# Kernel optimization log

Measured on AMD Instinct MI355X. Metric: run time of the kernel, lower is better.

Reference implementation:

```python
import jax, jax.numpy as jnp
import numpy as np

B, L, D, H, FF = 2, 4096, 512, 8, 2048
HD = D // H
EPS = 1e-5


def _layer_norm(x, g, b):
    mu = jnp.mean(x, axis=-1, keepdims=True)
    var = jnp.mean(jnp.square(x - mu), axis=-1, keepdims=True)
    return (x - mu) * jax.lax.rsqrt(var + EPS) * g + b


def setup_inputs() -> dict:
    key = jax.random.key(0)
    ks = jax.random.split(key, 16)
    s = 1.0 / np.sqrt(D)
    inp = {
        'x': jax.random.normal(ks[0], (B, L, D), dtype=jnp.float32),
        'Wq': jax.random.normal(ks[1], (D, D), dtype=jnp.float32) * s,
        'bq': jnp.zeros((D,), jnp.float32),
        'Wk': jax.random.normal(ks[2], (D, D), dtype=jnp.float32) * s,
        'bk': jnp.zeros((D,), jnp.float32),
        'Wv': jax.random.normal(ks[3], (D, D), dtype=jnp.float32) * s,
        'bv': jnp.zeros((D,), jnp.float32),
        'Wo': jax.random.normal(ks[4], (D, D), dtype=jnp.float32) * s,
        'bo': jnp.zeros((D,), jnp.float32),
        'ln1_g': jnp.ones((D,), jnp.float32),
        'ln1_b': jnp.zeros((D,), jnp.float32),
        'W1': jax.random.normal(ks[5], (D, FF), dtype=jnp.float32) * s,
        'b1': jnp.zeros((FF,), jnp.float32),
        'W2': jax.random.normal(ks[6], (FF, D), dtype=jnp.float32) * (1.0 / np.sqrt(FF)),
        'b2': jnp.zeros((D,), jnp.float32),
        'ln2_g': jnp.ones((D,), jnp.float32),
        'ln2_b': jnp.zeros((D,), jnp.float32),
        'window': 128,
    }
    return inp


def reference(x, Wq, bq, Wk, bk, Wv, bv, Wo, bo, ln1_g, ln1_b, W1, b1, W2, b2, ln2_g, ln2_b, window):
    # ---- local (banded) self-attention, matching nn.MultiheadAttention math ----
    q = (x @ Wq + bq).reshape(B, L, H, HD)
    k = (x @ Wk + bk).reshape(B, L, H, HD)
    v = (x @ Wv + bv).reshape(B, L, H, HD)
    scale = 1.0 / np.sqrt(HD)
    scores = jnp.einsum('bqhd,bkhd->bhqk', q, k) * scale  # [B,H,L,L]
    idx = jnp.arange(L)
    band = jnp.abs(idx[None, :] - idx[:, None]) > window   # True = masked
    scores = jnp.where(band[None, None], -jnp.inf, scores)
    probs = jax.nn.softmax(scores, axis=-1)
    attn = jnp.einsum('bhqk,bkhd->bqhd', probs, v).reshape(B, L, D)
    attn = attn @ Wo + bo
    # ---- residual + norm1 ----
    h = _layer_norm(x + attn, ln1_g, ln1_b)
    # ---- FFN + residual + norm2 (dropout=0 at eval) ----
    ff = jax.nn.relu(h @ W1 + b1) @ W2 + b2
    return _layer_norm(h + ff, ln2_g, ln2_b)
```

## Files before the change

kernel.cpp:

```cpp
#include <hip/hip_runtime.h>

namespace {

constexpr int B = 2, L = 4096, D = 512, H = 8, FF = 2048;
constexpr int M = B * L;
constexpr float LN_EPS = 1e-5f;

typedef __attribute__((ext_vector_type(8))) short short8;
typedef __attribute__((ext_vector_type(4))) float floatx4;

typedef __attribute__((address_space(3))) unsigned int lds_uint;
typedef const __attribute__((address_space(1))) unsigned int glob_uint;

__device__ __forceinline__ void gl_lds16(const unsigned short* g, unsigned short* l) {
  __builtin_amdgcn_global_load_lds((glob_uint*)g, (lds_uint*)l, 16, 0, 0);
}

__device__ __forceinline__ unsigned short f2bf(float f) {
  union { float f; unsigned u; } v; v.f = f;
  unsigned r = v.u + 0x7FFFu + ((v.u >> 16) & 1u);
  return (unsigned short)(r >> 16);
}

__device__ __forceinline__ float bf2f(unsigned short b) {
  union { unsigned u; float f; } v; v.u = ((unsigned)b) << 16;
  return v.f;
}

__global__ __launch_bounds__(256)
void k_prep(const float* __restrict__ x,
            const float* __restrict__ Wq, const float* __restrict__ Wk,
            const float* __restrict__ Wv, const float* __restrict__ Wo,
            const float* __restrict__ W1, const float* __restrict__ W2,
            const float* __restrict__ bq, const float* __restrict__ bk,
            const float* __restrict__ bv,
            unsigned short* __restrict__ Xb,
            unsigned short* __restrict__ WqkvT, unsigned short* __restrict__ WoT,
            unsigned short* __restrict__ W1T, unsigned short* __restrict__ W2T,
            float* __restrict__ bqkv) {
  __shared__ unsigned short tile[64 * 72];
  if (blockIdx.x < 4102) {
    int tid = blockIdx.x * blockDim.x + threadIdx.x;
    if (tid < 1048576) {
      float4 v = ((const float4*)x)[tid];
      ((ushort4*)Xb)[tid] = make_ushort4(f2bf(v.x), f2bf(v.y), f2bf(v.z), f2bf(v.w));
      return;
    }
    int u = tid - 1048576;
    if (u < 1536) bqkv[u] = (u < 512) ? bq[u] : (u < 1024 ? bk[u - 512] : bv[u - 1024]);
    return;
  }
  const int t = blockIdx.x - 4102;
  const float* src; unsigned short* dst; int Ns, Kd, n0, k0, nsrc0;
  if (t < 192) {
    int nt = t % 24, kt = t / 24; int ng = nt * 64;
    src = ng < 512 ? Wq : (ng < 1024 ? Wk : Wv);
    Ns = 512; Kd = 512; n0 = ng; nsrc0 = ng & 511; k0 = kt * 64; dst = WqkvT;
  } else if (t < 256) {
    int u = t - 192; int nt = u % 8, kt = u / 8;
    src = Wo; Ns = 512; Kd = 512; n0 = nt * 64; nsrc0 = n0; k0 = kt * 64; dst = WoT;
  } else if (t < 512) {
    int u = t - 256; int nt = u % 32, kt = u / 32;
    src = W1; Ns = 2048; Kd = 512; n0 = nt * 64; nsrc0 = n0; k0 = kt * 64; dst = W1T;
  } else {
    int u = t - 512; int nt = u % 8, kt = u / 8;
    src = W2; Ns = 512; Kd = 2048; n0 = nt * 64; nsrc0 = n0; k0 = kt * 64; dst = W2T;
  }
  const int tid = threadIdx.x;
  {
    int r = tid >> 2, cs = (tid & 3) * 16;
    const float4* sp = (const float4*)(src + (size_t)(k0 + r) * Ns + nsrc0 + cs);
    unsigned short* tp = &tile[r * 72 + cs];
#pragma unroll
    for (int i = 0; i < 4; ++i) {
      float4 v = sp[i];
      tp[i * 4 + 0] = f2bf(v.x); tp[i * 4 + 1] = f2bf(v.y);
      tp[i * 4 + 2] = f2bf(v.z); tp[i * 4 + 3] = f2bf(v.w);
    }
  }
  __syncthreads();
  {
    int n = tid >> 2, ks = (tid & 3) * 16;
    unsigned short buf[16];
#pragma unroll
    for (int e = 0; e < 16; ++e) buf[e] = tile[(ks + e) * 72 + n];
    unsigned short* dp = dst + (size_t)(n0 + n) * Kd + k0 + ks;
    *(short8*)dp = *(const short8*)&buf[0];
    *(short8*)(dp + 8) = *(const short8*)&buf[8];
  }
}

template <int EPI>
__global__ __launch_bounds__(256, 3)
void k_gemm(const unsigned short* __restrict__ A, const unsigned short* __restrict__ BT,
            const float* __restrict__ bias, void* __restrict__ Cout,
            unsigned short* __restrict__ Vout,
            const int klen, const int N) {
  __shared__ unsigned short lA[2][128 * 32];
  __shared__ unsigned short lB[2][128 * 32];
  unsigned flat = blockIdx.x + gridDim.x * (blockIdx.y + gridDim.y * blockIdx.z);
  const unsigned chunk = (gridDim.x * gridDim.y * gridDim.z) >> 3;
  flat = (flat & 7) * chunk + (flat >> 3);
  const unsigned bx = flat % gridDim.x;
  const unsigned rest = flat / gridDim.x;
  const unsigned by = rest % gridDim.y;
  const unsigned bz = rest / gridDim.y;

  const int tid = threadIdx.x;
  const int wave = tid >> 6, lane = tid & 63;
  const int quad = lane >> 4, l16 = lane & 15;
  const int m0 = by * 128, n0 = bx * 128;
  const int wm = (wave >> 1) * 64, wn = (wave & 1) * 64;
  const int kbeg = bz * klen;
  const size_t Kdim = (size_t)klen * gridDim.z;

  const floatx4 fzero = {0.f, 0.f, 0.f, 0.f};
  floatx4 acc[4][4];
#pragma unroll
  for (int i = 0; i < 4; ++i)
#pragma unroll
    for (int j = 0; j < 4; ++j) acc[i][j] = fzero;

  const int r0 = tid >> 2, o0 = (tid & 3) * 8;
  const int r1 = (256 + tid) >> 2, o1 = (tid & 3) * 8;
  const unsigned short* Ag0 = A + (size_t)(m0 + r0) * Kdim + kbeg + o0;
  const unsigned short* Ag1 = A + (size_t)(m0 + r1) * Kdim + kbeg + o1;
  const unsigned short* Bg0 = BT + (size_t)(n0 + r0) * Kdim + kbeg + o0;
  const unsigned short* Bg1 = BT + (size_t)(n0 + r1) * Kdim + kbeg + o1;

  auto stage = [&](int buf, int kt) {
    gl_lds16(Ag0 + kt, &lA[buf][wave * 512]);
    gl_lds16(Ag1 + kt, &lA[buf][(4 + wave) * 512]);
    gl_lds16(Bg0 + kt, &lB[buf][wave * 512]);
    gl_lds16(Bg1 + kt, &lB[buf][(4 + wave) * 512]);
  };

  stage(0, 0);
  __syncthreads();

  int buf = 0;
  for (int kt = 0; kt < klen; kt += 32, buf ^= 1) {
    if (kt + 32 < klen) stage(buf ^ 1, kt + 32);
    short8 af[4], bf[4];
#pragma unroll
    for (int i = 0; i < 4; ++i)
      af[i] = *(const short8*)&lA[buf][(wm + i * 16 + l16) * 32 + quad * 8];
#pragma unroll
    for (int j = 0; j < 4; ++j)
      bf[j] = *(const short8*)&lB[buf][(wn + j * 16 + l16) * 32 + quad * 8];
#pragma unroll
    for (int i = 0; i < 4; ++i)
#pragma unroll
      for (int j = 0; j < 4; ++j)
        acc[i][j] = __builtin_amdgcn_mfma_f32_16x16x32_bf16(af[i], bf[j], acc[i][j], 0, 0, 0);
    __syncthreads();
  }

  float* outf = (float*)Cout + (size_t)bz * M * N;
  const bool vblock = (EPI == 3) && (n0 >= 1024);
#pragma unroll
  for (int j = 0; j < 4; ++j) {
    const int col = n0 + wn + j * 16 + l16;
    const float bv = (bz == 0) ? bias[col] : 0.f;
#pragma unroll
    for (int i = 0; i < 4; ++i) {
      const int row = m0 + wm + i * 16 + quad * 4;
      if (EPI == 3 && vblock) {
        const int hh = (col - 1024) >> 6, dd = (col - 1024) & 63;
        const int bb = row >> 12, keyl = row & 4095;
        ushort4 pk = make_ushort4(f2bf(acc[i][j][0] + bv), f2bf(acc[i][j][1] + bv),
                                  f2bf(acc[i][j][2] + bv), f2bf(acc[i][j][3] + bv));
        *(ushort4*)(Vout + ((size_t)(bb * 8 + hh) * 64 + dd) * L + keyl) = pk;
      } else {
#pragma unroll
        for (int r = 0; r < 4; ++r) {
          float v = acc[i][j][r] + bv;
          if (EPI == 1) v = fmaxf(v, 0.f);
          if (EPI == 2)
            outf[(size_t)(row + r) * N + col] = v;
          else
            ((unsigned short*)Cout)[(size_t)(row + r) * N + col] = f2bf(v);
        }
      }
    }
  }
}

__global__ __launch_bounds__(256, 4)
void k_attn(const unsigned short* __restrict__ QKV, const unsigned short* __restrict__ Vg,
            unsigned short* __restrict__ attnb, const int* __restrict__ wptr) {
  const int W = wptr[0];
  __shared__ unsigned short Kt[2][4096];
  __shared__ unsigned short Vt[2][4096];
  const int tid = threadIdx.x;
  const int wave = tid >> 6, lane = tid & 63;
  const int quad = lane >> 4, l16 = lane & 15;
  const int bid = (int)((blockIdx.x & 7) * (gridDim.x >> 3) + (blockIdx.x >> 3));
  const int qt = bid & 63, h = (bid >> 6) & 7, b = bid >> 9;
  const int q0blk = qt * 64;
  const int q0 = q0blk + wave * 16;
  const float scale = 0.125f;

  const unsigned short* Kbase = QKV + (size_t)(b * L) * 1536 + 512 + h * 64;
  const unsigned short* Vh = Vg + (size_t)(b * 8 + h) * 64 * L;

  auto stage = [&](int buf, int jbg) {
#pragma unroll
    for (int i = 0; i < 2; ++i) {
      int c = i * 256 + tid;
      int kr = c >> 3;
      int key = jbg + kr;
      int keyc = key < 0 ? 0 : (key > L - 1 ? L - 1 : key);
      int dpart = (c & 7) ^ (kr & 7) ^ (((kr >> 3) & 3) << 1);
      gl_lds16(Kbase + (size_t)keyc * 1536 + dpart * 8,
               &Kt[buf][(i * 256 + wave * 64) * 8]);
    }
#pragma unroll
    for (int i = 0; i < 2; ++i) {
      int c = i * 256 + tid;
      int d = c >> 3;
      int kpart = (c & 7) ^ (d & 7);
      int kb = jbg + kpart * 8;
      kb = kb < 0 ? 0 : (kb > L - 8 ? L - 8 : kb);
      gl_lds16(Vh + (size_t)d * L + kb,
               &Vt[buf][(i * 256 + wave * 64) * 8]);
    }
  };

  const unsigned short* Qp = QKV + (size_t)(b * L + q0 + l16) * 1536 + h * 64;
  short8 qf0 = *(const short8*)(Qp + quad * 8);
  short8 qf1 = *(const short8*)(Qp + 32 + quad * 8);

  int koff[4][2];
#pragma unroll
  for (int tt = 0; tt < 4; ++tt) {
    int krow = (tt >> 1) * 32 + ((l16 >> 2) << 3) + (tt & 1) * 4 + (l16 & 3);
    int s2 = (krow & 7) ^ (((krow >> 3) & 3) << 1);
    koff[tt][0] = (krow * 8 + (quad ^ s2)) * 8;
    koff[tt][1] = (krow * 8 + ((quad + 4) ^ s2)) * 8;
  }
  int voff[4][2];
#pragma unroll
  for (int nt = 0; nt < 4; ++nt) {
    int d = nt * 16 + l16;
    voff[nt][0] = (d * 8 + (quad ^ (d & 7))) * 8;
    voff[nt][1] = (d * 8 + ((quad + 4) ^ (d & 7))) * 8;
  }

  const floatx4 fzero = {0.f, 0.f, 0.f, 0.f};
  floatx4 o[4];
#pragma unroll
  for (int i = 0; i < 4; ++i) o[i] = fzero;
  float lsum = 0.f;
  const int q = q0 + l16;

  stage(0, q0blk - 128);
  __syncthreads();

  for (int it = 0; it < 5; ++it) {
    const int jbg = q0blk - 128 + it * 64;
    if (it < 4) stage((it + 1) & 1, jbg + 64);
    const unsigned short* lk = Kt[it & 1];
    const unsigned short* lv = Vt[it & 1];
    const int dhi = q0 + 15 - jbg, dlo = jbg + 63 - q0;
    const bool fast = (jbg >= 0) && (jbg + 64 <= L) && ((dhi > dlo ? dhi : dlo) <= W);
    unsigned pu[8];
#pragma unroll
    for (int tt = 0; tt < 4; ++tt) {
      const short8 kf0 = *(const short8*)&lk[koff[tt][0]];
      const short8 kf1 = *(const short8*)&lk[koff[tt][1]];
      floatx4 z = fzero;
      z = __builtin_amdgcn_mfma_f32_16x16x32_bf16(kf0, qf0, z, 0, 0, 0);
      z = __builtin_amdgcn_mfma_f32_16x16x32_bf16(kf1, qf1, z, 0, 0, 0);
      float pv[4];
      if (fast) {
#pragma unroll
        for (int r = 0; r < 4; ++r) {
          float p = __expf(z[r] * scale);
          lsum += p;
          pv[r] = p;
        }
      } else {
        const int kb0 = jbg + (tt >> 1) * 32 + quad * 8 + (tt & 1) * 4;
#pragma unroll
        for (int r = 0; r < 4; ++r) {
          int key = kb0 + r;
          int dd = q - key; dd = dd < 0 ? -dd : dd;
          bool okk = (key >= 0) && (key < L) && (dd <= W);
          float p = okk ? __expf(z[r] * scale) : 0.f;
          lsum += p;
          pv[r] = p;
        }
      }
      unsigned lo, hi;
      asm("v_cvt_pk_bf16_f32 %0, %1, %2" : "=v"(lo) : "v"(pv[0]), "v"(pv[1]));
      asm("v_cvt_pk_bf16_f32 %0, %1, %2" : "=v"(hi) : "v"(pv[2]), "v"(pv[3]));
      pu[tt * 2 + 0] = lo;
      pu[tt * 2 + 1] = hi;
    }
    union { unsigned u[4]; short8 v; } pa0, pa1;
    pa0.u[0] = pu[0]; pa0.u[1] = pu[1]; pa0.u[2] = pu[2]; pa0.u[3] = pu[3];
    pa1.u[0] = pu[4]; pa1.u[1] = pu[5]; pa1.u[2] = pu[6]; pa1.u[3] = pu[7];
#pragma unroll
    for (int nt = 0; nt < 4; ++nt) {
      const short8 vf0 = *(const short8*)&lv[voff[nt][0]];
      const short8 vf1 = *(const short8*)&lv[voff[nt][1]];
      o[nt] = __builtin_amdgcn_mfma_f32_16x16x32_bf16(pa0.v, vf0, o[nt], 0, 0, 0);
      o[nt] = __builtin_amdgcn_mfma_f32_16x16x32_bf16(pa1.v, vf1, o[nt], 0, 0, 0);
    }
    __syncthreads();
  }
  lsum += __shfl_xor(lsum, 16, 64);
  lsum += __shfl_xor(lsum, 32, 64);
#pragma unroll
  for (int r = 0; r < 4; ++r) {
    float inv = 1.f / __shfl(lsum, quad * 4 + r, 64);
    size_t base = (size_t)(b * L + q0 + quad * 4 + r) * 512 + h * 64;
#pragma unroll
    for (int nt = 0; nt < 4; ++nt)
      attnb[base + nt * 16 + l16] = f2bf(o[nt][r] * inv);
  }
}

template <int RESBF>
__global__ __launch_bounds__(256, 2)
void k_res_ln(const float* __restrict__ t0, const float* __restrict__ t1,
              const void* __restrict__ res,
              const float* __restrict__ gamma, const float* __restrict__ beta,
              float* __restrict__ outf, unsigned short* __restrict__ outb) {
  const int wave = threadIdx.x >> 6, lane = threadIdx.x & 63;
  const int row = blockIdx.x * 4 + wave;
  const float4* tv = (const float4*)(t0 + (size_t)row * D);
  float4 a0 = tv[lane], a1 = tv[lane + 64];
  float4 b0, b1;
  if (RESBF) {
    const ushort4* rv = (const ushort4*)((const unsigned short*)res + (size_t)row * D);
    ushort4 u0 = rv[lane], u1 = rv[lane + 64];
    b0 = make_float4(bf2f(u0.x), bf2f(u0.y), bf2f(u0.z), bf2f(u0.w));
    b1 = make_float4(bf2f(u1.x), bf2f(u1.y), bf2f(u1.z), bf2f(u1.w));
  } else {
    const float4* rv = (const float4*)((const float*)res + (size_t)row * D);
    b0 = rv[lane]; b1 = rv[lane + 64];
  }
  float4 y0 = make_float4(a0.x + b0.x, a0.y + b0.y, a0.z + b0.z, a0.w + b0.w);
  float4 y1 = make_float4(a1.x + b1.x, a1.y + b1.y, a1.z + b1.z, a1.w + b1.w);
  {
    const float4* uv = (const float4*)(t1 + (size_t)row * D);
    float4 c0 = uv[lane], c1 = uv[lane + 64];
    y0.x += c0.x; y0.y += c0.y; y0.z += c0.z; y0.w += c0.w;
    y1.x += c1.x; y1.y += c1.y; y1.z += c1.z; y1.w += c1.w;
  }
  float s = y0.x + y0.y + y0.z + y0.w + y1.x + y1.y + y1.z + y1.w;
  float q = y0.x * y0.x + y0.y * y0.y + y0.z * y0.z + y0.w * y0.w +
            y1.x * y1.x + y1.y * y1.y + y1.z * y1.z + y1.w * y1.w;
#pragma unroll
  for (int d = 1; d < 64; d <<= 1) {
    s += __shfl_xor(s, d, 64);
    q += __shfl_xor(q, d, 64);
  }
  const float mean = s * (1.f / D);
  const float var = q * (1.f / D) - mean * mean;
  const float rstd = rsqrtf(var + LN_EPS);
  float4 g0 = ((const float4*)gamma)[lane], g1 = ((const float4*)gamma)[lane + 64];
  float4 e0 = ((const float4*)beta)[lane], e1 = ((const float4*)beta)[lane + 64];
  float4 o0 = make_float4((y0.x - mean) * rstd * g0.x + e0.x, (y0.y - mean) * rstd * g0.y + e0.y,
                          (y0.z - mean) * rstd * g0.z + e0.z, (y0.w - mean) * rstd * g0.w + e0.w);
  float4 o1 = make_float4((y1.x - mean) * rstd * g1.x + e1.x, (y1.y - mean) * rstd * g1.y + e1.y,
                          (y1.z - mean) * rstd * g1.z + e1.z, (y1.w - mean) * rstd * g1.w + e1.w);
  if (outf) {
    ((float4*)(outf + (size_t)row * D))[lane] = o0;
    ((float4*)(outf + (size_t)row * D))[lane + 64] = o1;
  }
  if (outb) {
    ((ushort4*)(outb + (size_t)row * D))[lane] =
        make_ushort4(f2bf(o0.x), f2bf(o0.y), f2bf(o0.z), f2bf(o0.w));
    ((ushort4*)(outb + (size_t)row * D))[lane + 64] =
        make_ushort4(f2bf(o1.x), f2bf(o1.y), f2bf(o1.z), f2bf(o1.w));
  }
}

}

extern "C" void kernel_launch(void* const* d_in, const int* in_sizes, int n_in,
                              void* d_out, int out_size, void* d_ws, size_t ws_size,
                              hipStream_t stream) {
  const float* x   = (const float*)d_in[0];
  const float* Wq  = (const float*)d_in[1];
  const float* bq  = (const float*)d_in[2];
  const float* Wk  = (const float*)d_in[3];
  const float* bk  = (const float*)d_in[4];
  const float* Wv  = (const float*)d_in[5];
  const float* bv  = (const float*)d_in[6];
  const float* Wo  = (const float*)d_in[7];
  const float* bo  = (const float*)d_in[8];
  const float* g1  = (const float*)d_in[9];
  const float* be1 = (const float*)d_in[10];
  const float* W1  = (const float*)d_in[11];
  const float* b1  = (const float*)d_in[12];
  const float* W2  = (const float*)d_in[13];
  const float* b2  = (const float*)d_in[14];
  const float* g2  = (const float*)d_in[15];
  const float* be2 = (const float*)d_in[16];
  const int* wptr  = (const int*)d_in[17];
  float* out = (float*)d_out;

  char* w = (char*)d_ws;
  size_t off = 0;
  auto take = [&](size_t bytes) -> void* {
    void* p = w + off;
    off += (bytes + 255) & ~(size_t)255;
    return p;
  };
  unsigned short* Xb    = (unsigned short*)take((size_t)M * D * 2);
  unsigned short* QKVb  = (unsigned short*)take((size_t)M * 1536 * 2);
  unsigned short* attnb = (unsigned short*)take((size_t)M * D * 2);
  unsigned short* Vg    = (unsigned short*)take((size_t)M * D * 2);
  unsigned short* WqkvT = (unsigned short*)take((size_t)1536 * 512 * 2);
  unsigned short* WoT   = (unsigned short*)take((size_t)512 * 512 * 2);
  unsigned short* W1T   = (unsigned short*)take((size_t)2048 * 512 * 2);
  unsigned short* W2T   = (unsigned short*)take((size_t)512 * 2048 * 2);
  float* bqkv           = (float*)take(1536 * 4);
  float* tbuf           = (float*)take((size_t)2 * M * D * 4);
  unsigned short* hb    = (unsigned short*)take((size_t)M * D * 2);
  unsigned short* ffb   = (unsigned short*)take((size_t)M * FF * 2);

  k_prep<<<4870, 256, 0, stream>>>(x, Wq, Wk, Wv, Wo, W1, W2, bq, bk, bv,
                                   Xb, WqkvT, WoT, W1T, W2T, bqkv);
  k_gemm<3><<<dim3(12, 64, 1), 256, 0, stream>>>(Xb, WqkvT, bqkv, QKVb, Vg, 512, 1536);
  k_attn<<<B * H * (L / 64), 256, 0, stream>>>(QKVb, Vg, attnb, wptr);
  k_gemm<2><<<dim3(4, 64, 2), 256, 0, stream>>>(attnb, WoT, bo, tbuf, nullptr, 256, 512);
  k_res_ln<0><<<M / 4, 256, 0, stream>>>(tbuf, tbuf + (size_t)M * D, x, g1, be1, nullptr, hb);
  k_gemm<1><<<dim3(16, 64, 1), 256, 0, stream>>>(hb, W1T, b1, ffb, nullptr, 512, 2048);
  k_gemm<2><<<dim3(4, 64, 2), 256, 0, stream>>>(ffb, W2T, b2, tbuf, nullptr, 1024, 512);
  k_res_ln<1><<<M / 4, 256, 0, stream>>>(tbuf, tbuf + (size_t)M * D, hb, g2, be2, out, nullptr);
}
```

Baseline: 233.7 us.

## Add 256x256-tile pipelined GEMM kernel for QKV and FFN1 projections

Adds a new GEMM kernel with 256x256 output tiles, 8 waves per block, and double-buffered direct global-to-LDS loads. Prefetches for the stage two steps ahead are interleaved between MFMA phases, and MFMA sections run at raised wave priority. The QKV and first FFN GEMMs switch from the 128-tile kernel to this one, which raises data reuse per loaded byte. The trade-off is fewer blocks (192 and 256) on a large-CU device, which risks poor occupancy and tail imbalance, plus heavy register pressure from the 8x4 accumulator array.

```diff
diff --git a/kernel.cpp b/kernel.cpp
--- a/kernel.cpp
+++ b/kernel.cpp
@@ -180,6 +180,158 @@
             outf[(size_t)(row + r) * N + col] = v;
           else
             ((unsigned short*)Cout)[(size_t)(row + r) * N + col] = f2bf(v);
+        }
+      }
+    }
+  }
+}
+
+template <int EPI>
+__global__ __launch_bounds__(512, 2)
+void k_gemm256(const unsigned short* __restrict__ A, const unsigned short* __restrict__ BT,
+               const float* __restrict__ bias, void* __restrict__ Cout,
+               unsigned short* __restrict__ Vout, const int NT, const int N) {
+  __shared__ unsigned short lds[2][2][256 * 64];
+  unsigned flat = blockIdx.x + gridDim.x * blockIdx.y;
+  const unsigned total = gridDim.x * gridDim.y;
+  flat = (flat & 7) * (total >> 3) + (flat >> 3);
+  const int bx = flat % gridDim.x, by = flat / gridDim.x;
+
+  const int tid = threadIdx.x;
+  const int wave = tid >> 6, lane = tid & 63;
+  const int quad = lane >> 4, l16 = lane & 15;
+  const int m0 = by * 256, n0 = bx * 256;
+  const int wm = (wave >> 2) * 128, wn = (wave & 3) * 64;
+  const size_t Kdim = (size_t)NT * 64;
+  const int swr = (l16 & 4) >> 1;
+
+  const floatx4 fzero = {0.f, 0.f, 0.f, 0.f};
+  floatx4 acc[8][4];
+#pragma unroll
+  for (int i = 0; i < 8; ++i)
+#pragma unroll
+    for (int j = 0; j < 4; ++j) acc[i][j] = fzero;
+
+  const int lsub = lane >> 3;
+  const int sg = (lane & 7) ^ ((lane >> 4) & 2);
+  const unsigned short* Ags = A + (size_t)(m0 + wave * 8 + lsub) * Kdim + sg * 8;
+  const unsigned short* Bgs = BT + (size_t)(n0 + wave * 8 + lsub) * Kdim + sg * 8;
+
+  auto stA = [&](int tt, int c) {
+    gl_lds16(Ags + (size_t)(c * 64) * Kdim + tt * 64,
+             &lds[tt & 1][0][(c * 64 + wave * 8) * 64]);
+  };
+  auto stB = [&](int tt, int c) {
+    gl_lds16(Bgs + (size_t)(c * 64) * Kdim + tt * 64,
+             &lds[tt & 1][1][(c * 64 + wave * 8) * 64]);
+  };
+
+  stA(0, 0); stA(0, 1); stA(0, 2); stA(0, 3);
+  stB(0, 0); stB(0, 1); stB(0, 2); stB(0, 3);
+  stA(1, 0); stA(1, 1); stA(1, 2); stA(1, 3);
+  stB(1, 0); stB(1, 1); stB(1, 2); stB(1, 3);
+  asm volatile("s_waitcnt vmcnt(8)" ::: "memory");
+  __builtin_amdgcn_s_barrier();
+
+  short8 aa[4][2], b0[2][2], b1[2][2];
+  for (int t = 0; t < NT; ++t) {
+    const unsigned short* la = &lds[t & 1][0][0];
+    const unsigned short* lb = &lds[t & 1][1][0];
+    const bool pf = (t + 2 < NT);
+#pragma unroll
+    for (int i = 0; i < 4; ++i)
+#pragma unroll
+      for (int kk = 0; kk < 2; ++kk)
+        aa[i][kk] = *(const short8*)&lds[t & 1][0]
+            [(wm + i * 16 + l16) * 64 + ((kk * 4 + quad) ^ swr) * 8];
+#pragma unroll
+    for (int j = 0; j < 2; ++j)
+#pragma unroll
+      for (int kk = 0; kk < 2; ++kk)
+        b0[j][kk] = *(const short8*)&lb[(wn + j * 16 + l16) * 64 + ((kk * 4 + quad) ^ swr) * 8];
+    __builtin_amdgcn_s_barrier();
+    __builtin_amdgcn_s_setprio(1);
+#pragma unroll
+    for (int i = 0; i < 4; ++i)
+#pragma unroll
+      for (int j = 0; j < 2; ++j) {
+        acc[i][j] = __builtin_amdgcn_mfma_f32_16x16x32_bf16(aa[i][0], b0[j][0], acc[i][j], 0, 0, 0);
+        acc[i][j] = __builtin_amdgcn_mfma_f32_16x16x32_bf16(aa[i][1], b0[j][1], acc[i][j], 0, 0, 0);
+      }
+    __builtin_amdgcn_s_setprio(0);
+    __builtin_amdgcn_s_barrier();
+#pragma unroll
+    for (int j = 0; j < 2; ++j)
+#pragma unroll
+      for (int kk = 0; kk < 2; ++kk)
+        b1[j][kk] = *(const short8*)&lb[(wn + 32 + j * 16 + l16) * 64 + ((kk * 4 + quad) ^ swr) * 8];
+    if (pf) { stA(t + 2, 0); stA(t + 2, 2); }
+    __builtin_amdgcn_s_barrier();
+    __builtin_amdgcn_s_setprio(1);
+#pragma unroll
+    for (int i = 0; i < 4; ++i)
+#pragma unroll
+      for (int j = 0; j < 2; ++j) {
+        acc[i][2 + j] = __builtin_amdgcn_mfma_f32_16x16x32_bf16(aa[i][0], b1[j][0], acc[i][2 + j], 0, 0, 0);
+        acc[i][2 + j] = __builtin_amdgcn_mfma_f32_16x16x32_bf16(aa[i][1], b1[j][1], acc[i][2 + j], 0, 0, 0);
+      }
+    __builtin_amdgcn_s_setprio(0);
+    __builtin_amdgcn_s_barrier();
+#pragma unroll
+    for (int i = 0; i < 4; ++i)
+#pragma unroll
+      for (int kk = 0; kk < 2; ++kk)
+        aa[i][kk] = *(const short8*)&lds[t & 1][0]
+            [(wm + 64 + i * 16 + l16) * 64 + ((kk * 4 + quad) ^ swr) * 8];
+    if (pf) { stB(t + 2, 0); stB(t + 2, 1); stB(t + 2, 2); stB(t + 2, 3); }
+    __builtin_amdgcn_s_barrier();
+    __builtin_amdgcn_s_setprio(1);
+#pragma unroll
+    for (int i = 0; i < 4; ++i)
+#pragma unroll
+      for (int j = 0; j < 2; ++j) {
+        acc[4 + i][j] = __builtin_amdgcn_mfma_f32_16x16x32_bf16(aa[i][0], b0[j][0], acc[4 + i][j], 0, 0, 0);
+        acc[4 + i][j] = __builtin_amdgcn_mfma_f32_16x16x32_bf16(aa[i][1], b0[j][1], acc[4 + i][j], 0, 0, 0);
+      }
+    __builtin_amdgcn_s_setprio(0);
+    __builtin_amdgcn_s_barrier();
+    if (pf) { stA(t + 2, 1); stA(t + 2, 3); }
+    __builtin_amdgcn_s_barrier();
+    __builtin_amdgcn_s_setprio(1);
+#pragma unroll
+    for (int i = 0; i < 4; ++i)
+#pragma unroll
+      for (int j = 0; j < 2; ++j) {
+        acc[4 + i][2 + j] = __builtin_amdgcn_mfma_f32_16x16x32_bf16(aa[i][0], b1[j][0], acc[4 + i][2 + j], 0, 0, 0);
+        acc[4 + i][2 + j] = __builtin_amdgcn_mfma_f32_16x16x32_bf16(aa[i][1], b1[j][1], acc[4 + i][2 + j], 0, 0, 0);
+      }
+    __builtin_amdgcn_s_setprio(0);
+    if (pf) asm volatile("s_waitcnt vmcnt(8)" ::: "memory");
+    else if (t + 1 < NT) asm volatile("s_waitcnt vmcnt(0)" ::: "memory");
+    __builtin_amdgcn_s_barrier();
+  }
+
+  unsigned short* outb = (unsigned short*)Cout;
+  const bool vblock = (EPI == 3) && (n0 >= 1024);
+#pragma unroll
+  for (int j = 0; j < 4; ++j) {
+    const int col = n0 + wn + j * 16 + l16;
+    const float bv = bias[col];
+#pragma unroll
+    for (int i = 0; i < 8; ++i) {
+      const int row = m0 + wm + i * 16 + quad * 4;
+      if (EPI == 3 && vblock) {
+        const int hh = (col - 1024) >> 6, dd = (col - 1024) & 63;
+        const int bb = row >> 12, keyl = row & 4095;
+        ushort4 pk = make_ushort4(f2bf(acc[i][j][0] + bv), f2bf(acc[i][j][1] + bv),
+                                  f2bf(acc[i][j][2] + bv), f2bf(acc[i][j][3] + bv));
+        *(ushort4*)(Vout + ((size_t)(bb * 8 + hh) * 64 + dd) * L + keyl) = pk;
+      } else {
+#pragma unroll
+        for (int r = 0; r < 4; ++r) {
+          float v = acc[i][j][r] + bv;
+          if (EPI == 1) v = fmaxf(v, 0.f);
+          outb[(size_t)(row + r) * N + col] = f2bf(v);
         }
       }
     }
@@ -426,11 +578,11 @@
 
   k_prep<<<4870, 256, 0, stream>>>(x, Wq, Wk, Wv, Wo, W1, W2, bq, bk, bv,
                                    Xb, WqkvT, WoT, W1T, W2T, bqkv);
-  k_gemm<3><<<dim3(12, 64, 1), 256, 0, stream>>>(Xb, WqkvT, bqkv, QKVb, Vg, 512, 1536);
+  k_gemm256<3><<<dim3(6, 32), 512, 0, stream>>>(Xb, WqkvT, bqkv, QKVb, Vg, 8, 1536);
   k_attn<<<B * H * (L / 64), 256, 0, stream>>>(QKVb, Vg, attnb, wptr);
   k_gemm<2><<<dim3(4, 64, 2), 256, 0, stream>>>(attnb, WoT, bo, tbuf, nullptr, 256, 512);
   k_res_ln<0><<<M / 4, 256, 0, stream>>>(tbuf, tbuf + (size_t)M * D, x, g1, be1, nullptr, hb);
-  k_gemm<1><<<dim3(16, 64, 1), 256, 0, stream>>>(hb, W1T, b1, ffb, nullptr, 512, 2048);
+  k_gemm256<1><<<dim3(8, 32), 512, 0, stream>>>(hb, W1T, b1, ffb, nullptr, 8, 2048);
   k_gemm<2><<<dim3(4, 64, 2), 256, 0, stream>>>(ffb, W2T, b2, tbuf, nullptr, 1024, 512);
   k_res_ln<1><<<M / 4, 256, 0, stream>>>(tbuf, tbuf + (size_t)M * D, hb, g2, be2, out, nullptr);
 }
```

New measurement: 237.1 us. About the same (+1.5%).
